# Kernel tuning notes

Hardware: AMD Instinct MI355X
Metric: run time of the kernel (lower is better)

Reference implementation:

```python
import jax, jax.numpy as jnp
import numpy as np
from jax import lax

EPS = 1e-5

def _rsign(x, beta):
    # per-channel learnable shift followed by sign binarization
    return jnp.sign(x + beta[None, :, None, None])

def _scaled_sign_conv(x, w, stride, pad):
    # XNOR-style binarized weights: sign(W) * mean(|W|) per output filter
    alpha = jnp.mean(jnp.abs(w), axis=(1, 2, 3), keepdims=True)
    wb = jnp.sign(w) * alpha
    return lax.conv_general_dilated(x, wb, (stride, stride), [(pad, pad), (pad, pad)],
                                    dimension_numbers=('NCHW', 'OIHW', 'NCHW'))

def _bn(x, gamma, beta):
    # training-mode batch norm (batch statistics), matching torch default forward
    m = jnp.mean(x, axis=(0, 2, 3), keepdims=True)
    v = jnp.var(x, axis=(0, 2, 3), keepdims=True)
    xn = (x - m) * lax.rsqrt(v + EPS)
    return xn * gamma[None, :, None, None] + beta[None, :, None, None]

def _rprelu(x, gamma, zeta, slope):
    g = gamma[None, :, None, None]
    s = slope[None, :, None, None]
    xs = x - g
    return jnp.where(xs > 0, xs, s * xs) + zeta[None, :, None, None]

def _avgpool2(x):
    B, C, H, W = x.shape
    return x.reshape(B, C, H // 2, 2, W // 2, 2).mean(axis=(3, 5))

def reference(x, rsign1_beta, w1, bn1_gamma, bn1_beta, rsign2_beta, w2, bn2_gamma, bn2_beta, pr_gamma, pr_zeta, pr_slope):
    # layer1: RSign -> 3x3 stride-2 scaled_sign conv -> BN
    out1 = _bn(_scaled_sign_conv(_rsign(x, rsign1_beta), w1, 2, 1), bn1_gamma, bn1_beta)
    out1 = out1 + _avgpool2(x)
    out1 = _rprelu(out1, pr_gamma, pr_zeta, pr_slope)
    # layer2 (shared weights, called twice with identical inputs -> identical outputs)
    out2 = _bn(_scaled_sign_conv(_rsign(out1, rsign2_beta), w2, 1, 0), bn2_gamma, bn2_beta)
    y = out2 + out1
    return jnp.concatenate([y, y], axis=1)

def setup_inputs() -> dict:
    key = jax.random.key(0)
    ks = jax.random.split(key, 8)
    B, C, H, W = 32, 256, 56, 56
    return {
        'x': jax.random.normal(ks[0], (B, C, H, W), jnp.float32),
        'rsign1_beta': jax.random.normal(ks[1], (C,), jnp.float32) * 0.1,
        'w1': jax.random.normal(ks[2], (C, C, 3, 3), jnp.float32) * 0.05,
        'bn1_gamma': jnp.ones((C,), jnp.float32),
        'bn1_beta': jnp.zeros((C,), jnp.float32),
        'rsign2_beta': jax.random.normal(ks[3], (C,), jnp.float32) * 0.1,
        'w2': jax.random.normal(ks[4], (C, C, 1, 1), jnp.float32) * 0.05,
        'bn2_gamma': jnp.ones((C,), jnp.float32),
        'bn2_beta': jnp.zeros((C,), jnp.float32),
        'pr_gamma': jax.random.normal(ks[5], (C,), jnp.float32) * 0.1,
        'pr_zeta': jax.random.normal(ks[6], (C,), jnp.float32) * 0.1,
        'pr_slope': jnp.full((C,), 0.25, jnp.float32),
    }
```

## Files before the change

### kernel.cpp

```cpp
#include <hip/hip_runtime.h>
#include <stdint.h>

typedef unsigned long long u64;
typedef uint32_t u32;

#define BB  32
#define CC  256
#define HH  56
#define WW  56
#define OHH 28
#define OWW 28
#define NPIX (BB*OHH*OWW)
#define PACKBLKS 3136
#define FGRID (BB*OHH)

__global__ __launch_bounds__(256) void rrb_prep_pack(const float* __restrict__ x,
                                                     const float* __restrict__ rsb1,
                                                     const float* __restrict__ w1,
                                                     const float* __restrict__ w2,
                                                     u32* __restrict__ xb, float* __restrict__ pool,
                                                     u32* __restrict__ wp1, u32* __restrict__ wp2,
                                                     float* __restrict__ alpha1, float* __restrict__ alpha2,
                                                     u32* __restrict__ stats_zero, int* __restrict__ bar) {
    if (blockIdx.x >= PACKBLKS) {
        __shared__ float red[256];
        int pb = blockIdx.x - PACKBLKS;
        int co = pb & 255;
        int t = threadIdx.x;
        int wid = t >> 6, lane = t & 63;
        if (pb == 0) {
            #pragma unroll
            for (int k = 0; k < 6; ++k) stats_zero[k * 256 + t] = 0u;
            if (t == 0) *bar = 0;
        }
        float asum = 0.f;
        if (pb < 256) {
            const float* wr = w1 + (size_t)co * 2304 + (size_t)t * 9;
            float v[9];
            #pragma unroll
            for (int k = 0; k < 9; ++k) { v[k] = wr[k]; asum += fabsf(v[k]); }
            #pragma unroll
            for (int k = 0; k < 9; ++k) {
                u64 m = __ballot(v[k] > 0.f);
                if (lane == 0)
                    *(u64*)&wp1[((size_t)co * 9 + k) * 8 + 2 * wid] = m;
            }
        } else {
            float v = w2[co * 256 + t];
            asum = fabsf(v);
            u64 m = __ballot(v > 0.f);
            if (lane == 0) *(u64*)&wp2[co * 8 + 2 * wid] = m;
        }
        red[t] = asum; __syncthreads();
        for (int st = 128; st > 0; st >>= 1) {
            if (t < st) red[t] += red[t + st];
            __syncthreads();
        }
        if (t == 0) {
            if (pb < 256) alpha1[co] = red[0] / 2304.f;
            else          alpha2[co] = red[0] / 256.f;
        }
        return;
    }
    int i = blockIdx.x * 256 + threadIdx.x;
    int s  = i & 3;
    int i2 = i >> 2;
    int ow = i2 % OWW;
    int i3 = i2 / OWW;
    int oh = i3 % OHH;
    int i4 = i3 / OHH;
    int n  = i4 & 31;
    int j  = i4 >> 5;
    int c0 = 32 * j + 8 * s;
    const float* base = x + (((size_t)(n * CC + c0) * HH + 2 * oh) * WW + 2 * ow);

    float2 a0[8], a1[8];
    #pragma unroll
    for (int cc = 0; cc < 8; ++cc) {
        const float* p = base + (size_t)cc * (HH * WW);
        a0[cc] = *(const float2*)p;
        a1[cc] = *(const float2*)(p + WW);
    }
    float4 b0 = *(const float4*)&rsb1[c0];
    float4 b1 = *(const float4*)&rsb1[c0 + 4];

    u32 w00 = 0, w01 = 0, w10 = 0, w11 = 0;
    float pv[8];
    #pragma unroll
    for (int cc = 0; cc < 8; ++cc) {
        float b = (cc < 4) ? ((const float*)&b0)[cc] : ((const float*)&b1)[cc - 4];
        w00 |= (u32)(a0[cc].x + b > 0.f) << cc;
        w01 |= (u32)(a0[cc].y + b > 0.f) << cc;
        w10 |= (u32)(a1[cc].x + b > 0.f) << cc;
        w11 |= (u32)(a1[cc].y + b > 0.f) << cc;
        pv[cc] = (a0[cc].x + a0[cc].y + a1[cc].x + a1[cc].y) * 0.25f;
    }
    w00 <<= 8 * s; w01 <<= 8 * s; w10 <<= 8 * s; w11 <<= 8 * s;
    w00 |= __shfl_xor(w00, 1); w00 |= __shfl_xor(w00, 2);
    w01 |= __shfl_xor(w01, 1); w01 |= __shfl_xor(w01, 2);
    w10 |= __shfl_xor(w10, 1); w10 |= __shfl_xor(w10, 2);
    w11 |= __shfl_xor(w11, 1); w11 |= __shfl_xor(w11, 2);

    float* pp = pool + ((size_t)(n * OHH + oh) * OWW + ow) * CC + c0;
    *(float4*)&pp[0] = make_float4(pv[0], pv[1], pv[2], pv[3]);
    *(float4*)&pp[4] = make_float4(pv[4], pv[5], pv[6], pv[7]);

    u32* xo = xb + (((size_t)(n * HH + 2 * oh) * WW + 2 * ow) * 8) + j;
    u32 wsel = (s == 0) ? w00 : (s == 1) ? w01 : (s == 2) ? w10 : w11;
    int off = (s == 0) ? 0 : (s == 1) ? 8 : (s == 2) ? WW * 8 : WW * 8 + 8;
    xo[off] = wsel;
}

__device__ __forceinline__ void gbar(int* cnt, int target) {
    __syncthreads();
    if (threadIdx.x == 0) {
        __hip_atomic_fetch_add(cnt, 1, __ATOMIC_RELAXED, __HIP_MEMORY_SCOPE_AGENT);
        int guard = 0;
        while (__hip_atomic_load(cnt, __ATOMIC_RELAXED, __HIP_MEMORY_SCOPE_AGENT) < target) {
            __builtin_amdgcn_s_sleep(16);
            if (++guard > (1 << 22)) break;
        }
    }
    __syncthreads();
}

__device__ __forceinline__ void bn_fold_v(int sv, u64 qv, float al_, float g_, float be_,
                                          float& a, float& b) {
    const double N = (double)NPIX;
    double s = (double)sv;
    double q = (double)qv;
    double mS = s / N;
    double vS = q / N - mS * mS;
    double al = (double)al_;
    double scale = (double)g_ / sqrt(al * al * vS + 1e-5);
    a = (float)(al * scale);
    b = (float)((double)be_ - al * mS * scale);
}

__global__ __launch_bounds__(256, 4) void rrb_fused(const u32* __restrict__ xb,
                                                    const u32* __restrict__ wp1,
                                                    const u32* __restrict__ wp2,
                                                    const float* __restrict__ pool,
                                                    int* __restrict__ st1_sum, u64* __restrict__ st1_sq,
                                                    int* __restrict__ st2_sum, u64* __restrict__ st2_sq,
                                                    const float* __restrict__ alpha1,
                                                    const float* __restrict__ bn1g, const float* __restrict__ bn1b,
                                                    const float* __restrict__ alpha2,
                                                    const float* __restrict__ bn2g, const float* __restrict__ bn2b,
                                                    const float* __restrict__ pg, const float* __restrict__ pz,
                                                    const float* __restrict__ ps, const float* __restrict__ rsb2,
                                                    float* __restrict__ y, int* __restrict__ bar) {
    __shared__ char shraw[256 * 29 * 4 + OWW * 8 * 4];
    u32*   xs   = (u32*)shraw;
    float* tb   = (float*)shraw;
    u32*   bits = (u32*)(shraw + 256 * 29 * 4);

    int blk = blockIdx.x;
    int n = blk / OHH, oh = blk - n * OHH;
    int c = threadIdx.x;
    int wid = c >> 6, lane = c & 63;

    int r0 = 2 * oh - 1;
    for (int i = c; i < 3 * WW * 8; i += 256) {
        int row = i / (WW * 8);
        int ih = r0 + row;
        xs[i] = (ih >= 0) ? xb[((size_t)(n * HH + ih) * WW) * 8 + (i - row * WW * 8)] : 0u;
    }
    u32 svp[14];
    {
        u32 wreg[72];
        const u32* wsrc = wp1 + (size_t)c * 72;
        #pragma unroll
        for (int i = 0; i < 72; ++i) wreg[i] = wsrc[i];
        __syncthreads();
        bool oh0 = (oh == 0);
        int bsum = 0; long long bsq = 0;
        #pragma unroll
        for (int ow = 0; ow < OWW; ++ow) {
            int S = 0;
            #pragma unroll
            for (int kh = 0; kh < 3; ++kh) {
                bool vkh = !(kh == 0 && oh0);
                #pragma unroll
                for (int kw = 0; kw < 3; ++kw) {
                    int iw = 2 * ow + kw - 1;
                    bool ok = vkh && (iw >= 0);
                    int iwc = iw < 0 ? 0 : iw;
                    const u32* xp = &xs[(kh * WW + iwc) * 8];
                    int p = 0;
                    #pragma unroll
                    for (int j = 0; j < 8; ++j) p += __popc(xp[j] ^ wreg[(kh * 3 + kw) * 8 + j]);
                    S += ok ? (256 - 2 * p) : 0;
                }
            }
            if ((ow & 1) == 0) svp[ow >> 1] = (u32)(S & 0xffff);
            else               svp[ow >> 1] |= (u32)(S & 0xffff) << 16;
            bsum += S;
            bsq += (long long)S * S;
        }
        int o1 = atomicAdd(&st1_sum[c], bsum);
        u64 o2 = atomicAdd(&st1_sq[c], (u64)bsq);
        asm volatile("" :: "v"(o1), "v"((u32)o2), "v"((u32)(o2 >> 32)));
    }

    gbar(bar, FGRID);

    float ov[OWW];
    u32 wr2[8];
    {
        int s1v = __hip_atomic_load(&st1_sum[c], __ATOMIC_RELAXED, __HIP_MEMORY_SCOPE_AGENT);
        u64 q1v = __hip_atomic_load(&st1_sq[c], __ATOMIC_RELAXED, __HIP_MEMORY_SCOPE_AGENT);
        float a1, b1;
        bn_fold_v(s1v, q1v, alpha1[c], bn1g[c], bn1b[c], a1, b1);
        float g = pg[c], z = pz[c], sl = ps[c], b2 = rsb2[c];
        const float* pp = pool + ((size_t)(n * OHH + oh) * OWW) * CC + c;
        #pragma unroll
        for (int k = 0; k < OWW; ++k) {
            int S = (k & 1) ? (((int)svp[k >> 1]) >> 16)
                            : (((int)(svp[k >> 1] << 16)) >> 16);
            float v = a1 * (float)S + b1 + pp[k * CC];
            float xsv = v - g;
            float o = (xsv > 0.f ? xsv : sl * xsv) + z;
            ov[k] = o;
            u64 m = __ballot(o + b2 > 0.f);
            if (lane == 0) *(u64*)&bits[k * 8 + 2 * wid] = m;
        }
        const u32* wsv = wp2 + (size_t)c * 8;
        #pragma unroll
        for (int j = 0; j < 8; ++j) wr2[j] = wsv[j];
        __syncthreads();
        int bsum = 0; long long bsq = 0;
        #pragma unroll
        for (int k = 0; k < OWW; ++k) {
            int p = 0;
            #pragma unroll
            for (int j = 0; j < 8; ++j) p += __popc(bits[k * 8 + j] ^ wr2[j]);
            int S = 256 - 2 * p;
            bsum += S;
            bsq += (long long)S * S;
        }
        int o1 = atomicAdd(&st2_sum[c], bsum);
        u64 o2 = atomicAdd(&st2_sq[c], (u64)bsq);
        asm volatile("" :: "v"(o1), "v"((u32)o2), "v"((u32)(o2 >> 32)));
    }

    gbar(bar, 2 * FGRID);

    {
        int s2v = __hip_atomic_load(&st2_sum[c], __ATOMIC_RELAXED, __HIP_MEMORY_SCOPE_AGENT);
        u64 q2v = __hip_atomic_load(&st2_sq[c], __ATOMIC_RELAXED, __HIP_MEMORY_SCOPE_AGENT);
        float a2, b2f;
        bn_fold_v(s2v, q2v, alpha2[c], bn2g[c], bn2b[c], a2, b2f);
        #pragma unroll
        for (int ow = 0; ow < OWW; ++ow) {
            int p = 0;
            #pragma unroll
            for (int j = 0; j < 8; ++j) p += __popc(bits[ow * 8 + j] ^ wr2[j]);
            int S = 256 - 2 * p;
            tb[c * 29 + ow] = a2 * (float)S + b2f + ov[ow];
        }
        __syncthreads();
        #pragma unroll
        for (int it = 0; it < 7; ++it) {
            int idx = it * 256 + c;
            int cp = idx / 7, qq = idx - cp * 7;
            const float* lp = &tb[cp * 29 + 4 * qq];
            float4 v = make_float4(lp[0], lp[1], lp[2], lp[3]);
            float* dst = y + ((size_t)(n * 2 * CC + cp) * OHH + oh) * OWW + 4 * qq;
            *(float4*)dst = v;
            *(float4*)(dst + (size_t)CC * OHH * OWW) = v;
        }
    }
}

extern "C" void kernel_launch(void* const* d_in, const int* in_sizes, int n_in,
                              void* d_out, int out_size, void* d_ws, size_t ws_size,
                              hipStream_t stream) {
    const float* x    = (const float*)d_in[0];
    const float* rsb1 = (const float*)d_in[1];
    const float* w1   = (const float*)d_in[2];
    const float* bn1g = (const float*)d_in[3];
    const float* bn1b = (const float*)d_in[4];
    const float* rsb2 = (const float*)d_in[5];
    const float* w2   = (const float*)d_in[6];
    const float* bn2g = (const float*)d_in[7];
    const float* bn2b = (const float*)d_in[8];
    const float* pg   = (const float*)d_in[9];
    const float* pz   = (const float*)d_in[10];
    const float* ps   = (const float*)d_in[11];
    float* y = (float*)d_out;

    char* ws = (char*)d_ws;
    if (ws_size < 28995584) return;

    u32*   wp1    = (u32*)(ws + 0);
    u32*   wp2    = (u32*)(ws + 73728);
    float* alpha1 = (float*)(ws + 81920);
    float* alpha2 = (float*)(ws + 82944);
    int*   bar     = (int*)(ws + 84992);
    int*   st1_sum = (int*)(ws + 88064);
    u64*   st1_sq  = (u64*)(ws + 89088);
    int*   st2_sum = (int*)(ws + 91136);
    u64*   st2_sq  = (u64*)(ws + 92160);
    u32*   xb   = (u32*)(ws + 94208);
    float* pool = (float*)(ws + 3305472);

    u32* stats_zero = (u32*)(ws + 88064);

    rrb_prep_pack<<<PACKBLKS + 512, 256, 0, stream>>>(x, rsb1, w1, w2, xb, pool,
                                                      wp1, wp2, alpha1, alpha2,
                                                      stats_zero, bar);
    rrb_fused<<<FGRID, 256, 0, stream>>>(xb, wp1, wp2, pool,
                                         st1_sum, st1_sq, st2_sum, st2_sq,
                                         alpha1, bn1g, bn1b, alpha2, bn2g, bn2b,
                                         pg, pz, ps, rsb2, y, bar);
}
```

Before: 175.7 us.

## Replace per-channel global atomics with per-block partials and distributed BN reduction

Each block now writes its per-channel sum and sum-of-squares partials to dedicated workspace slots instead of doing contended atomicAdds on 256 shared counters. After a grid barrier, the first 256 blocks each reduce one channel's partials and publish folded BN scale/shift. Two extra grid barriers are then needed per BN stage. The intent is to remove atomic contention (896 blocks hitting the same addresses). The cost is extra barriers and partial-buffer traffic, and the sum of squares is truncated to 32 bits per block.

```diff
diff --git a/kernel.cpp b/kernel.cpp
--- a/kernel.cpp
+++ b/kernel.cpp
@@ -21,18 +21,14 @@
                                                      u32* __restrict__ xb, float* __restrict__ pool,
                                                      u32* __restrict__ wp1, u32* __restrict__ wp2,
                                                      float* __restrict__ alpha1, float* __restrict__ alpha2,
-                                                     u32* __restrict__ stats_zero, int* __restrict__ bar) {
+                                                     int* __restrict__ bar) {
     if (blockIdx.x >= PACKBLKS) {
         __shared__ float red[256];
         int pb = blockIdx.x - PACKBLKS;
         int co = pb & 255;
         int t = threadIdx.x;
         int wid = t >> 6, lane = t & 63;
-        if (pb == 0) {
-            #pragma unroll
-            for (int k = 0; k < 6; ++k) stats_zero[k * 256 + t] = 0u;
-            if (t == 0) *bar = 0;
-        }
+        if (pb == 0 && t == 0) *bar = 0;
         float asum = 0.f;
         if (pb < 256) {
             const float* wr = w1 + (size_t)co * 2304 + (size_t)t * 9;
@@ -118,13 +114,13 @@
         int guard = 0;
         while (__hip_atomic_load(cnt, __ATOMIC_RELAXED, __HIP_MEMORY_SCOPE_AGENT) < target) {
             __builtin_amdgcn_s_sleep(16);
-            if (++guard > (1 << 22)) break;
+            if (++guard > (1 << 20)) break;
         }
     }
     __syncthreads();
 }
 
-__device__ __forceinline__ void bn_fold_v(int sv, u64 qv, float al_, float g_, float be_,
+__device__ __forceinline__ void bn_fold_v(long long sv, u64 qv, float al_, float g_, float be_,
                                           float& a, float& b) {
     const double N = (double)NPIX;
     double s = (double)sv;
@@ -137,12 +133,17 @@
     b = (float)((double)be_ - al * mS * scale);
 }
 
+#define AST(p, v)  __hip_atomic_store((p), (v), __ATOMIC_RELAXED, __HIP_MEMORY_SCOPE_AGENT)
+#define ALD(p)     __hip_atomic_load((p), __ATOMIC_RELAXED, __HIP_MEMORY_SCOPE_AGENT)
+
 __global__ __launch_bounds__(256, 4) void rrb_fused(const u32* __restrict__ xb,
                                                     const u32* __restrict__ wp1,
                                                     const u32* __restrict__ wp2,
                                                     const float* __restrict__ pool,
-                                                    int* __restrict__ st1_sum, u64* __restrict__ st1_sq,
-                                                    int* __restrict__ st2_sum, u64* __restrict__ st2_sq,
+                                                    int* __restrict__ P1s, u32* __restrict__ P1q,
+                                                    int* __restrict__ P2s, u32* __restrict__ P2q,
+                                                    u32* __restrict__ A1, u32* __restrict__ B1,
+                                                    u32* __restrict__ A2, u32* __restrict__ B2,
                                                     const float* __restrict__ alpha1,
                                                     const float* __restrict__ bn1g, const float* __restrict__ bn1b,
                                                     const float* __restrict__ alpha2,
@@ -151,9 +152,11 @@
                                                     const float* __restrict__ ps, const float* __restrict__ rsb2,
                                                     float* __restrict__ y, int* __restrict__ bar) {
     __shared__ char shraw[256 * 29 * 4 + OWW * 8 * 4];
-    u32*   xs   = (u32*)shraw;
-    float* tb   = (float*)shraw;
-    u32*   bits = (u32*)(shraw + 256 * 29 * 4);
+    u32*       xs   = (u32*)shraw;
+    float*     tb   = (float*)shraw;
+    long long* redS = (long long*)shraw;
+    long long* redQ = (long long*)(shraw + 2048);
+    u32*       bits = (u32*)(shraw + 256 * 29 * 4);
 
     int blk = blockIdx.x;
     int n = blk / OHH, oh = blk - n * OHH;
@@ -198,20 +201,41 @@
             bsum += S;
             bsq += (long long)S * S;
         }
-        int o1 = atomicAdd(&st1_sum[c], bsum);
-        u64 o2 = atomicAdd(&st1_sq[c], (u64)bsq);
-        asm volatile("" :: "v"(o1), "v"((u32)o2), "v"((u32)(o2 >> 32)));
+        AST(&P1s[blk * 256 + c], bsum);
+        AST(&P1q[blk * 256 + c], (u32)bsq);
+        asm volatile("s_waitcnt vmcnt(0)" ::: "memory");
     }
 
     gbar(bar, FGRID);
+
+    if (blk < 256) {
+        int r = blk;
+        long long aS = 0, aQ = 0;
+        for (int k = c; k < FGRID; k += 256) {
+            aS += (long long)(int)ALD(&P1s[k * 256 + r]);
+            aQ += (long long)(u64)ALD(&P1q[k * 256 + r]);
+        }
+        redS[c] = aS; redQ[c] = aQ; __syncthreads();
+        for (int st = 128; st > 0; st >>= 1) {
+            if (c < st) { redS[c] += redS[c + st]; redQ[c] += redQ[c + st]; }
+            __syncthreads();
+        }
+        if (c == 0) {
+            float a, b;
+            bn_fold_v(redS[0], (u64)redQ[0], alpha1[r], bn1g[r], bn1b[r], a, b);
+            AST(&A1[r], __float_as_uint(a));
+            AST(&B1[r], __float_as_uint(b));
+            asm volatile("s_waitcnt vmcnt(0)" ::: "memory");
+        }
+    }
+
+    gbar(bar, 2 * FGRID);
 
     float ov[OWW];
     u32 wr2[8];
     {
-        int s1v = __hip_atomic_load(&st1_sum[c], __ATOMIC_RELAXED, __HIP_MEMORY_SCOPE_AGENT);
-        u64 q1v = __hip_atomic_load(&st1_sq[c], __ATOMIC_RELAXED, __HIP_MEMORY_SCOPE_AGENT);
-        float a1, b1;
-        bn_fold_v(s1v, q1v, alpha1[c], bn1g[c], bn1b[c], a1, b1);
+        float a1 = __uint_as_float(ALD(&A1[c]));
+        float b1 = __uint_as_float(ALD(&B1[c]));
         float g = pg[c], z = pz[c], sl = ps[c], b2 = rsb2[c];
         const float* pp = pool + ((size_t)(n * OHH + oh) * OWW) * CC + c;
         #pragma unroll
@@ -239,26 +263,50 @@
             bsum += S;
             bsq += (long long)S * S;
         }
-        int o1 = atomicAdd(&st2_sum[c], bsum);
-        u64 o2 = atomicAdd(&st2_sq[c], (u64)bsq);
-        asm volatile("" :: "v"(o1), "v"((u32)o2), "v"((u32)(o2 >> 32)));
-    }
-
-    gbar(bar, 2 * FGRID);
+        AST(&P2s[blk * 256 + c], bsum);
+        AST(&P2q[blk * 256 + c], (u32)bsq);
+        asm volatile("s_waitcnt vmcnt(0)" ::: "memory");
+    }
+
+    gbar(bar, 3 * FGRID);
+
+    if (blk < 256) {
+        int r = blk;
+        long long aS = 0, aQ = 0;
+        for (int k = c; k < FGRID; k += 256) {
+            aS += (long long)(int)ALD(&P2s[k * 256 + r]);
+            aQ += (long long)(u64)ALD(&P2q[k * 256 + r]);
+        }
+        redS[c] = aS; redQ[c] = aQ; __syncthreads();
+        for (int st = 128; st > 0; st >>= 1) {
+            if (c < st) { redS[c] += redS[c + st]; redQ[c] += redQ[c + st]; }
+            __syncthreads();
+        }
+        if (c == 0) {
+            float a, b;
+            bn_fold_v(redS[0], (u64)redQ[0], alpha2[r], bn2g[r], bn2b[r], a, b);
+            AST(&A2[r], __float_as_uint(a));
+            AST(&B2[r], __float_as_uint(b));
+            asm volatile("s_waitcnt vmcnt(0)" ::: "memory");
+        }
+    }
+
+    gbar(bar, 4 * FGRID);
 
     {
-        int s2v = __hip_atomic_load(&st2_sum[c], __ATOMIC_RELAXED, __HIP_MEMORY_SCOPE_AGENT);
-        u64 q2v = __hip_atomic_load(&st2_sq[c], __ATOMIC_RELAXED, __HIP_MEMORY_SCOPE_AGENT);
-        float a2, b2f;
-        bn_fold_v(s2v, q2v, alpha2[c], bn2g[c], bn2b[c], a2, b2f);
+        float a2  = __uint_as_float(ALD(&A2[c]));
+        float b2f = __uint_as_float(ALD(&B2[c]));
+        float sv2[OWW];
         #pragma unroll
         for (int ow = 0; ow < OWW; ++ow) {
             int p = 0;
             #pragma unroll
             for (int j = 0; j < 8; ++j) p += __popc(bits[ow * 8 + j] ^ wr2[j]);
-            int S = 256 - 2 * p;
-            tb[c * 29 + ow] = a2 * (float)S + b2f + ov[ow];
-        }
+            sv2[ow] = a2 * (float)(256 - 2 * p) + b2f + ov[ow];
+        }
+        __syncthreads();
+        #pragma unroll
+        for (int ow = 0; ow < OWW; ++ow) tb[c * 29 + ow] = sv2[ow];
         __syncthreads();
         #pragma unroll
         for (int it = 0; it < 7; ++it) {
@@ -291,27 +339,28 @@
     float* y = (float*)d_out;
 
     char* ws = (char*)d_ws;
-    if (ws_size < 28995584) return;
+    if (ws_size < 32665600) return;
 
     u32*   wp1    = (u32*)(ws + 0);
     u32*   wp2    = (u32*)(ws + 73728);
     float* alpha1 = (float*)(ws + 81920);
     float* alpha2 = (float*)(ws + 82944);
-    int*   bar     = (int*)(ws + 84992);
-    int*   st1_sum = (int*)(ws + 88064);
-    u64*   st1_sq  = (u64*)(ws + 89088);
-    int*   st2_sum = (int*)(ws + 91136);
-    u64*   st2_sq  = (u64*)(ws + 92160);
+    int*   bar    = (int*)(ws + 84992);
+    u32*   A1     = (u32*)(ws + 86016);
+    u32*   B1     = (u32*)(ws + 87040);
+    u32*   A2     = (u32*)(ws + 88064);
+    u32*   B2     = (u32*)(ws + 89088);
     u32*   xb   = (u32*)(ws + 94208);
     float* pool = (float*)(ws + 3305472);
-
-    u32* stats_zero = (u32*)(ws + 88064);
+    int*   P1s  = (int*)(ws + 28995584);
+    u32*   P1q  = (u32*)(ws + 29913088);
+    int*   P2s  = (int*)(ws + 30830592);
+    u32*   P2q  = (u32*)(ws + 31748096);
 
     rrb_prep_pack<<<PACKBLKS + 512, 256, 0, stream>>>(x, rsb1, w1, w2, xb, pool,
-                                                      wp1, wp2, alpha1, alpha2,
-                                                      stats_zero, bar);
+                                                      wp1, wp2, alpha1, alpha2, bar);
     rrb_fused<<<FGRID, 256, 0, stream>>>(xb, wp1, wp2, pool,
-                                         st1_sum, st1_sq, st2_sum, st2_sq,
+                                         P1s, P1q, P2s, P2q, A1, B1, A2, B2,
                                          alpha1, bn1g, bn1b, alpha2, bn2g, bn2b,
                                          pg, pz, ps, rsb2, y, bar);
 }
```

After: 282.7 us. 60.9% more time.
